# Optimization experiments

Measured on AMD Instinct MI355X. Metric: run time of the kernel, lower is better.

The kernel has to match this reference:

```python
import jax, jax.numpy as jnp
import numpy as np

# 1x1 conv (bias=False) + BatchNorm (eval mode, running mean=0, var=1 -> per-channel
# affine scale/shift, matching SyncBN at init/inference) + ReLU
def _cbr(x, W, g, b):
    y = jnp.einsum('bchw,oc->bohw', x, W)
    y = y * g[None, :, None, None] + b[None, :, None, None]
    return jax.nn.relu(y)


def setup_inputs() -> dict:
    key = jax.random.key(0)
    ks = jax.random.split(key, 8)
    B, C, H, Wd = 4, 512, 64, 64   # batch, feats_channels, spatial
    Ct = 256                        # transform_channels
    Ck = 2 * C                      # key_in_channels = feats_channels * 2

    def w(k, o, i):
        return jax.random.normal(k, (o, i), jnp.float32) * (1.0 / np.sqrt(i))

    inp = {"x": jax.random.normal(ks[0], (B, C, H, Wd), jnp.float32)}
    # query_project: two conv+BN+ReLU blocks, C -> Ct -> Ct
    inp["qW1"] = w(ks[1], Ct, C);  inp["qg1"] = jnp.ones((Ct,), jnp.float32); inp["qb1"] = jnp.zeros((Ct,), jnp.float32)
    inp["qW2"] = w(ks[2], Ct, Ct); inp["qg2"] = jnp.ones((Ct,), jnp.float32); inp["qb2"] = jnp.zeros((Ct,), jnp.float32)
    # key_project: two conv+BN+ReLU blocks, 2C -> Ct -> Ct
    inp["kW1"] = w(ks[3], Ct, Ck); inp["kg1"] = jnp.ones((Ct,), jnp.float32); inp["kb1"] = jnp.zeros((Ct,), jnp.float32)
    inp["kW2"] = w(ks[4], Ct, Ct); inp["kg2"] = jnp.ones((Ct,), jnp.float32); inp["kb2"] = jnp.zeros((Ct,), jnp.float32)
    # value_project: one conv+BN+ReLU, 2C -> Ct
    inp["vW"] = w(ks[5], Ct, Ck);  inp["vg"] = jnp.ones((Ct,), jnp.float32);  inp["vb"] = jnp.zeros((Ct,), jnp.float32)
    # out_project: one conv+BN+ReLU, Ct -> C
    inp["oW"] = w(ks[6], C, Ct);   inp["og"] = jnp.ones((C,), jnp.float32);   inp["ob"] = jnp.zeros((C,), jnp.float32)
    return inp


def reference(x, qW1, qg1, qb1, qW2, qg2, qb2,
              kW1, kg1, kb1, kW2, kg2, kb2,
              vW, vg, vb, oW, og, ob):
    B, C, H, W = x.shape
    # global avgpool to 1x1, bilinear-upsample back to HxW == broadcast of the mean
    xg = jnp.broadcast_to(jnp.mean(x, axis=(2, 3), keepdims=True), (B, C, H, W))
    key_feats = jnp.concatenate([xg, x], axis=1)  # [B, 2C, H, W]

    q = _cbr(_cbr(x, qW1, qg1, qb1), qW2, qg2, qb2)          # [B, Ct, H, W]
    k = _cbr(_cbr(key_feats, kW1, kg1, kb1), kW2, kg2, kb2)  # [B, Ct, H, W]
    v = _cbr(key_feats, vW, vg, vb)                          # [B, Ct, H, W]

    Ct = q.shape[1]
    HW = H * W
    qf = q.reshape(B, Ct, HW).transpose(0, 2, 1)  # [B, HW, Ct]
    kf = k.reshape(B, Ct, HW)                     # [B, Ct, HW]
    vf = v.reshape(B, Ct, HW).transpose(0, 2, 1)  # [B, HW, Ct]

    sim = jnp.einsum('bnc,bcm->bnm', qf, kf) * (Ct ** -0.5)  # [B, HW, HW]
    attn = jax.nn.softmax(sim, axis=-1)
    ctx = jnp.einsum('bnm,bmc->bnc', attn, vf)               # [B, HW, Ct]
    ctx = ctx.transpose(0, 2, 1).reshape(B, Ct, H, W)

    return _cbr(ctx, oW, og, ob)  # [B, C, H, W]
```

## Files before the change

### kernel.cpp

```cpp
#include <hip/hip_runtime.h>
#include <stdint.h>

typedef __bf16 bf16x8 __attribute__((ext_vector_type(8)));
typedef float f32x4 __attribute__((ext_vector_type(4)));
typedef unsigned short u16;
typedef uint32_t u32;

union V16 { uint4 v; u16 e[8]; };

__device__ __forceinline__ float bf2f(u16 h) {
    u32 u = ((u32)h) << 16; float f; __builtin_memcpy(&f, &u, 4); return f;
}
__device__ __forceinline__ u16 f2bf(float f) {
    u32 u; __builtin_memcpy(&u, &f, 4);
    u32 r = (u + 0x7FFFu + ((u >> 16) & 1u)) >> 16; return (u16)r;
}
__device__ __forceinline__ u32 cvtpk(float lo, float hi) {
    u32 r;
    asm("v_cvt_pk_bf16_f32 %0, %1, %2" : "=v"(r) : "v"(lo), "v"(hi));
    return r;
}
__device__ __forceinline__ f32x4 mfma16(bf16x8 a, bf16x8 b, f32x4 c) {
    return __builtin_amdgcn_mfma_f32_16x16x32_bf16(a, b, c, 0, 0, 0);
}
__device__ __forceinline__ void gll16(const u16* g, u16* l) {
    __builtin_amdgcn_global_load_lds(
        (const __attribute__((address_space(1))) unsigned int*)g,
        (__attribute__((address_space(3))) unsigned int*)l, 16, 0, 0);
}
__device__ __forceinline__ float loadElem(const void* p, size_t i, int fl) {
    if (fl == 1) return ((const float*)p)[i];
    if (fl == 2) return (float)((const double*)p)[i];
    return bf2f(((const u16*)p)[i]);
}

__global__ __launch_bounds__(256) void k_detect(const u32* __restrict__ xw, int* __restrict__ flag) {
    int t = threadIdx.x;
    int cA = 0, cB = 0;
    #pragma unroll
    for (int i = 0; i < 16; i++) {
        u32 w = xw[i * 256 + t];
        cA += (((w >> 23) & 0xFFu) >= 0xC0u) ? 1 : 0;
        cB += (((w >> 7)  & 0xFFu) >= 0xC0u) ? 1 : 0;
    }
    #pragma unroll
    for (int m = 32; m >= 1; m >>= 1) { cA += __shfl_xor(cA, m); cB += __shfl_xor(cB, m); }
    __shared__ int sA[4], sB[4];
    if ((t & 63) == 0) { sA[t >> 6] = cA; sB[t >> 6] = cB; }
    __syncthreads();
    if (t == 0) {
        int a = sA[0] + sA[1] + sA[2] + sA[3];
        int b = sB[0] + sB[1] + sB[2] + sB[3];
        *flag = (a > 64) ? 2 : ((b > 64) ? 1 : 0);
    }
}

__global__ __launch_bounds__(256) void k_xpose(const void* __restrict__ xv, const int* __restrict__ dt,
                                               u16* __restrict__ xT, float* __restrict__ partial) {
    __shared__ u16 tile[64][72];
    int b = blockIdx.z;
    int n0 = blockIdx.x * 64, c0 = blockIdx.y * 64;
    u16* xTb = xT + (size_t)b * 4096 * 512;
    int t = threadIdx.x;
    int fl = *dt;
    const size_t xbase = (size_t)b * 512 * 4096;
    if (fl == 1) {
        const float* xb = (const float*)xv + xbase;
        int cr = t >> 4, n4 = (t & 15) * 4;
        #pragma unroll
        for (int i = 0; i < 4; i++) {
            int c = cr + i * 16;
            float4 v = *reinterpret_cast<const float4*>(xb + (size_t)(c0 + c) * 4096 + n0 + n4);
            tile[n4 + 0][c] = f2bf(v.x); tile[n4 + 1][c] = f2bf(v.y);
            tile[n4 + 2][c] = f2bf(v.z); tile[n4 + 3][c] = f2bf(v.w);
            float s = (v.x + v.y) + (v.z + v.w);
            s += __shfl_xor(s, 1); s += __shfl_xor(s, 2);
            s += __shfl_xor(s, 4); s += __shfl_xor(s, 8);
            if ((t & 15) == 0)
                partial[((size_t)b * 512 + c0 + c) * 64 + blockIdx.x] = s;
        }
    } else {
        int c4 = t >> 6, n = t & 63;
        for (int i = 0; i < 16; i++) {
            int c = c4 + i * 4;
            float v = loadElem(xv, xbase + (size_t)(c0 + c) * 4096 + n0 + n, fl);
            tile[n][c] = f2bf(v);
            float s = v;
            #pragma unroll
            for (int m = 32; m >= 1; m >>= 1) s += __shfl_xor(s, m);
            if (n == 0)
                partial[((size_t)b * 512 + c0 + c) * 64 + blockIdx.x] = s;
        }
    }
    __syncthreads();
    int nr = t >> 3, c8 = (t & 7) * 8;
    #pragma unroll
    for (int i = 0; i < 2; i++) {
        int n = nr + i * 32;
        V16 v;
        #pragma unroll
        for (int j = 0; j < 8; j++) v.e[j] = tile[n][c8 + j];
        *reinterpret_cast<uint4*>(xTb + (size_t)(n0 + n) * 512 + c0 + c8) = v.v;
    }
}

__global__ __launch_bounds__(256) void k_mean2(const float* __restrict__ partial, float* __restrict__ xg) {
    int bc = blockIdx.x * 256 + threadIdx.x;
    const float* p = partial + (size_t)bc * 64;
    float s = 0.f;
    #pragma unroll
    for (int i = 0; i < 64; i++) s += p[i];
    xg[bc] = s * (1.f / 4096.f);
}

__global__ __launch_bounds__(64) void k_consts(const void* __restrict__ kW1, const void* __restrict__ vW,
                                               const int* __restrict__ dt, const float* __restrict__ xg,
                                               float* __restrict__ ck, float* __restrict__ cv) {
    int bo = blockIdx.x; int b = bo >> 8; int o = bo & 255;
    int l = threadIdx.x;
    int fl = *dt;
    const float* g = xg + b * 512;
    float sk = 0.f, sv = 0.f;
    for (int c = l; c < 512; c += 64) {
        float xv = g[c];
        sk += loadElem(kW1, (size_t)o * 1024 + c, fl) * xv;
        sv += loadElem(vW,  (size_t)o * 1024 + c, fl) * xv;
    }
    #pragma unroll
    for (int m = 32; m >= 1; m >>= 1) { sk += __shfl_xor(sk, m); sv += __shfl_xor(sv, m); }
    if (l == 0) { ck[bo] = sk; cv[bo] = sv; }
}

__global__ __launch_bounds__(256) void k_wconv(const void* __restrict__ qW1, const void* __restrict__ qW2,
                                               const void* __restrict__ kW1, const void* __restrict__ kW2,
                                               const void* __restrict__ vW, const void* __restrict__ oW,
                                               const int* __restrict__ dt, u16* __restrict__ dst) {
    int i = blockIdx.x * 256 + threadIdx.x;
    int fl = *dt;
    const void* s; size_t so;
    if (i < 131072)      { s = qW1; so = (size_t)i; }
    else if (i < 196608) { int j = i - 131072; s = qW2; so = (size_t)j; }
    else if (i < 327680) { int j = i - 196608; s = kW1; so = (size_t)(j >> 9) * 1024 + 512 + (j & 511); }
    else if (i < 393216) { int j = i - 327680; s = kW2; so = (size_t)j; }
    else if (i < 524288) { int j = i - 393216; s = vW;  so = (size_t)(j >> 9) * 1024 + 512 + (j & 511); }
    else                 { int j = i - 524288; s = oW;  so = (size_t)j; }
    dst[i] = f2bf(loadElem(s, so, fl));
}

__global__ __launch_bounds__(256) void k_pconv(const void* qg1, const void* qb1, const void* qg2, const void* qb2,
                                               const void* kg1, const void* kb1, const void* kg2, const void* kb2,
                                               const void* vg, const void* vb, const void* og, const void* ob,
                                               const int* __restrict__ dt, float* __restrict__ pg) {
    int j = blockIdx.x * 256 + threadIdx.x;
    if (j >= 3584) return;
    int fl = *dt;
    const void* s; int o;
    if (j < 256)       { s = qg1; o = j; }
    else if (j < 512)  { s = qb1; o = j - 256; }
    else if (j < 768)  { s = qg2; o = j - 512; }
    else if (j < 1024) { s = qb2; o = j - 768; }
    else if (j < 1280) { s = kg1; o = j - 1024; }
    else if (j < 1536) { s = kb1; o = j - 1280; }
    else if (j < 1792) { s = kg2; o = j - 1536; }
    else if (j < 2048) { s = kb2; o = j - 1792; }
    else if (j < 2304) { s = vg;  o = j - 2048; }
    else if (j < 2560) { s = vb;  o = j - 2304; }
    else if (j < 3072) { s = og;  o = j - 2560; }
    else               { s = ob;  o = j - 3072; }
    pg[j] = loadElem(s, (size_t)o, fl);
}

template<bool AFF_ROW, typename OT>
__global__ __launch_bounds__(256) void k_gemm_bt(
    const u16* __restrict__ A, long aBS, int lda,
    const u16* __restrict__ Bm, long bBS, int ldb,
    OT* __restrict__ C, long cBS, int ldc,
    const float* __restrict__ gamma, const float* __restrict__ beta,
    const float* __restrict__ bias, int biasBS, int K) {
    __shared__ u16 As[2][128 * 64];
    __shared__ u16 Bs[2][128 * 64];
    int b = blockIdx.z;
    const u16* Ab = A + (size_t)b * aBS;
    const u16* Bb = Bm + (size_t)b * bBS;
    OT* Cb = C + (size_t)b * cBS;
    int m0 = blockIdx.x * 128, n0 = blockIdx.y * 128;
    int t = threadIdx.x;
    int lane = t & 63, wid = t >> 6;
    int wr = wid >> 1, wc = wid & 1;
    int li = lane & 15, lk = lane >> 4;

    f32x4 acc[4][4] = {};

    auto stage = [&](int k0, int buf) {
        #pragma unroll
        for (int j = 0; j < 4; j++) {
            int c = wid * 4 + j;
            u32 pl = (u32)c * 1024 + (u32)lane * 16;
            u32 r = pl >> 7;
            u32 q = (pl & 127) ^ ((r & 7) << 4);
            gll16(Ab + (size_t)(m0 + r) * lda + k0 + (q >> 1), &As[buf][0] + (c << 9));
            gll16(Bb + (size_t)(n0 + r) * ldb + k0 + (q >> 1), &Bs[buf][0] + (c << 9));
        }
    };

    const int nk = K >> 6;
    stage(0, 0);

    for (int kst = 0; kst < nk; kst++) {
        int cur = kst & 1;
        if (kst + 1 < nk) {
            stage((kst + 1) << 6, cur ^ 1);
            asm volatile("s_waitcnt vmcnt(8)" ::: "memory");
        } else {
            asm volatile("s_waitcnt vmcnt(0)" ::: "memory");
        }
        __builtin_amdgcn_sched_barrier(0);
        __builtin_amdgcn_s_barrier();

        const char* AsB = (const char*)&As[cur][0];
        const char* BsB = (const char*)&Bs[cur][0];
        #pragma unroll
        for (int ks = 0; ks < 2; ks++) {
            bf16x8 af[4], bfr[4];
            #pragma unroll
            for (int mi = 0; mi < 4; mi++) {
                int r = wr * 64 + mi * 16 + li;
                u32 off = ((u32)(r * 128 + (ks * 32 + lk * 8) * 2)) ^ (((u32)(r & 7)) << 4);
                af[mi] = *reinterpret_cast<const bf16x8*>(AsB + off);
            }
            #pragma unroll
            for (int ni = 0; ni < 4; ni++) {
                int r = wc * 64 + ni * 16 + li;
                u32 off = ((u32)(r * 128 + (ks * 32 + lk * 8) * 2)) ^ (((u32)(r & 7)) << 4);
                bfr[ni] = *reinterpret_cast<const bf16x8*>(BsB + off);
            }
            #pragma unroll
            for (int mi = 0; mi < 4; mi++)
                #pragma unroll
                for (int ni = 0; ni < 4; ni++)
                    acc[mi][ni] = mfma16(af[mi], bfr[ni], acc[mi][ni]);
        }
        asm volatile("s_waitcnt lgkmcnt(0)" ::: "memory");
        __builtin_amdgcn_s_barrier();
    }
    #pragma unroll
    for (int mi = 0; mi < 4; mi++) {
        #pragma unroll
        for (int ni = 0; ni < 4; ni++) {
            #pragma unroll
            for (int r = 0; r < 4; r++) {
                int m = m0 + wr * 64 + mi * 16 + lk * 4 + r;
                int n = n0 + wc * 64 + ni * 16 + li;
                int oc = AFF_ROW ? m : n;
                float v = acc[mi][ni][r];
                if (bias) v += bias[b * biasBS + oc];
                float y = v * gamma[oc] + beta[oc];
                y = fmaxf(y, 0.f);
                if constexpr (sizeof(OT) == 2) Cb[(size_t)m * ldc + n] = f2bf(y);
                else                           Cb[(size_t)m * ldc + n] = y;
            }
        }
    }
}

__global__ __launch_bounds__(256) void k_gemm_tri(
    const u16* __restrict__ xT, long xBS,
    const u16* __restrict__ Wq, const u16* __restrict__ Wk, const u16* __restrict__ Wv,
    u16* __restrict__ Cq, u16* __restrict__ Ck2, u16* __restrict__ Cv, long cBS,
    const float* __restrict__ pg, const float* __restrict__ ckb, const float* __restrict__ cvb) {
    __shared__ u16 As[2][128 * 64];
    __shared__ u16 Bs[2][128 * 64];
    int z = blockIdx.z;
    int op = z >> 2, b = z & 3;
    const u16* Ab; const u16* Bb; u16* Cb; int ldc;
    const float* gamma; const float* beta; const float* bias;
    int m0, n0;
    if (op == 2) {
        Ab = Wv; Bb = xT + (size_t)b * xBS; Cb = Cv + (size_t)b * cBS; ldc = 4096;
        gamma = pg + 2048; beta = pg + 2304; bias = cvb;
        m0 = blockIdx.y * 128; n0 = blockIdx.x * 128;
    } else if (op == 1) {
        Ab = xT + (size_t)b * xBS; Bb = Wk; Cb = Ck2 + (size_t)b * cBS; ldc = 256;
        gamma = pg + 1024; beta = pg + 1280; bias = ckb;
        m0 = blockIdx.x * 128; n0 = blockIdx.y * 128;
    } else {
        Ab = xT + (size_t)b * xBS; Bb = Wq; Cb = Cq + (size_t)b * cBS; ldc = 256;
        gamma = pg + 0; beta = pg + 256; bias = nullptr;
        m0 = blockIdx.x * 128; n0 = blockIdx.y * 128;
    }
    int t = threadIdx.x;
    int lane = t & 63, wid = t >> 6;
    int wr = wid >> 1, wc = wid & 1;
    int li = lane & 15, lk = lane >> 4;

    f32x4 acc[4][4] = {};

    auto stage = [&](int k0, int buf) {
        #pragma unroll
        for (int j = 0; j < 4; j++) {
            int c = wid * 4 + j;
            u32 pl = (u32)c * 1024 + (u32)lane * 16;
            u32 r = pl >> 7;
            u32 q = (pl & 127) ^ ((r & 7) << 4);
            gll16(Ab + (size_t)(m0 + r) * 512 + k0 + (q >> 1), &As[buf][0] + (c << 9));
            gll16(Bb + (size_t)(n0 + r) * 512 + k0 + (q >> 1), &Bs[buf][0] + (c << 9));
        }
    };

    stage(0, 0);

    for (int kst = 0; kst < 8; kst++) {
        int cur = kst & 1;
        if (kst + 1 < 8) {
            stage((kst + 1) << 6, cur ^ 1);
            asm volatile("s_waitcnt vmcnt(8)" ::: "memory");
        } else {
            asm volatile("s_waitcnt vmcnt(0)" ::: "memory");
        }
        __builtin_amdgcn_sched_barrier(0);
        __builtin_amdgcn_s_barrier();

        const char* AsB = (const char*)&As[cur][0];
        const char* BsB = (const char*)&Bs[cur][0];
        #pragma unroll
        for (int ks = 0; ks < 2; ks++) {
            bf16x8 af[4], bfr[4];
            #pragma unroll
            for (int mi = 0; mi < 4; mi++) {
                int r = wr * 64 + mi * 16 + li;
                u32 off = ((u32)(r * 128 + (ks * 32 + lk * 8) * 2)) ^ (((u32)(r & 7)) << 4);
                af[mi] = *reinterpret_cast<const bf16x8*>(AsB + off);
            }
            #pragma unroll
            for (int ni = 0; ni < 4; ni++) {
                int r = wc * 64 + ni * 16 + li;
                u32 off = ((u32)(r * 128 + (ks * 32 + lk * 8) * 2)) ^ (((u32)(r & 7)) << 4);
                bfr[ni] = *reinterpret_cast<const bf16x8*>(BsB + off);
            }
            #pragma unroll
            for (int mi = 0; mi < 4; mi++)
                #pragma unroll
                for (int ni = 0; ni < 4; ni++)
                    acc[mi][ni] = mfma16(af[mi], bfr[ni], acc[mi][ni]);
        }
        asm volatile("s_waitcnt lgkmcnt(0)" ::: "memory");
        __builtin_amdgcn_s_barrier();
    }
    #pragma unroll
    for (int mi = 0; mi < 4; mi++) {
        #pragma unroll
        for (int ni = 0; ni < 4; ni++) {
            #pragma unroll
            for (int r = 0; r < 4; r++) {
                int m = m0 + wr * 64 + mi * 16 + lk * 4 + r;
                int n = n0 + wc * 64 + ni * 16 + li;
                int oc = (op == 2) ? m : n;
                float v = acc[mi][ni][r];
                if (bias) v += bias[b * 256 + oc];
                float y = v * gamma[oc] + beta[oc];
                y = fmaxf(y, 0.f);
                Cb[(size_t)m * ldc + n] = f2bf(y);
            }
        }
    }
}

__global__ __launch_bounds__(256) void k_gemm_pair(
    const u16* __restrict__ A0, const u16* __restrict__ A1, long aBS, int lda,
    const u16* __restrict__ B0, const u16* __restrict__ B1, int ldb,
    u16* __restrict__ C0, u16* __restrict__ C1, long cBS, int ldc,
    const float* __restrict__ g0, const float* __restrict__ be0,
    const float* __restrict__ g1, const float* __restrict__ be1, int K) {
    __shared__ u16 As[2][128 * 64];
    __shared__ u16 Bs[2][128 * 64];
    int z = blockIdx.z;
    int op = z >> 2, b = z & 3;
    const u16* Ab = (op ? A1 : A0) + (size_t)b * aBS;
    const u16* Bb = op ? B1 : B0;
    u16* Cb = (op ? C1 : C0) + (size_t)b * cBS;
    const float* gamma = op ? g1 : g0;
    const float* beta  = op ? be1 : be0;
    int m0 = blockIdx.x * 128, n0 = blockIdx.y * 128;
    int t = threadIdx.x;
    int lane = t & 63, wid = t >> 6;
    int wr = wid >> 1, wc = wid & 1;
    int li = lane & 15, lk = lane >> 4;

    f32x4 acc[4][4] = {};

    auto stage = [&](int k0, int buf) {
        #pragma unroll
        for (int j = 0; j < 4; j++) {
            int c = wid * 4 + j;
            u32 pl = (u32)c * 1024 + (u32)lane * 16;
            u32 r = pl >> 7;
            u32 q = (pl & 127) ^ ((r & 7) << 4);
            gll16(Ab + (size_t)(m0 + r) * lda + k0 + (q >> 1), &As[buf][0] + (c << 9));
            gll16(Bb + (size_t)(n0 + r) * ldb + k0 + (q >> 1), &Bs[buf][0] + (c << 9));
        }
    };

    const int nk = K >> 6;
    stage(0, 0);

    for (int kst = 0; kst < nk; kst++) {
        int cur = kst & 1;
        if (kst + 1 < nk) {
            stage((kst + 1) << 6, cur ^ 1);
            asm volatile("s_waitcnt vmcnt(8)" ::: "memory");
        } else {
            asm volatile("s_waitcnt vmcnt(0)" ::: "memory");
        }
        __builtin_amdgcn_sched_barrier(0);
        __builtin_amdgcn_s_barrier();

        const char* AsB = (const char*)&As[cur][0];
        const char* BsB = (const char*)&Bs[cur][0];
        #pragma unroll
        for (int ks = 0; ks < 2; ks++) {
            bf16x8 af[4], bfr[4];
            #pragma unroll
            for (int mi = 0; mi < 4; mi++) {
                int r = wr * 64 + mi * 16 + li;
                u32 off = ((u32)(r * 128 + (ks * 32 + lk * 8) * 2)) ^ (((u32)(r & 7)) << 4);
                af[mi] = *reinterpret_cast<const bf16x8*>(AsB + off);
            }
            #pragma unroll
            for (int ni = 0; ni < 4; ni++) {
                int r = wc * 64 + ni * 16 + li;
                u32 off = ((u32)(r * 128 + (ks * 32 + lk * 8) * 2)) ^ (((u32)(r & 7)) << 4);
                bfr[ni] = *reinterpret_cast<const bf16x8*>(BsB + off);
            }
            #pragma unroll
            for (int mi = 0; mi < 4; mi++)
                #pragma unroll
                for (int ni = 0; ni < 4; ni++)
                    acc[mi][ni] = mfma16(af[mi], bfr[ni], acc[mi][ni]);
        }
        asm volatile("s_waitcnt lgkmcnt(0)" ::: "memory");
        __builtin_amdgcn_s_barrier();
    }
    #pragma unroll
    for (int mi = 0; mi < 4; mi++) {
        #pragma unroll
        for (int ni = 0; ni < 4; ni++) {
            #pragma unroll
            for (int r = 0; r < 4; r++) {
                int m = m0 + wr * 64 + mi * 16 + lk * 4 + r;
                int n = n0 + wc * 64 + ni * 16 + li;
                float v = acc[mi][ni][r];
                float y = v * gamma[n] + beta[n];
                y = fmaxf(y, 0.f);
                Cb[(size_t)m * ldc + n] = f2bf(y);
            }
        }
    }
}

__global__ __launch_bounds__(256, 2) void k_attn(const u16* __restrict__ Q, const u16* __restrict__ Kt,
                                                 const u16* __restrict__ V, u16* __restrict__ Op,
                                                 float2* __restrict__ ML) {
    __shared__ u16 Ks[2][32 * 256];
    __shared__ u16 Vs[2][256 * 32];
    __shared__ u16 Ps[128 * 32];
    char* PsB = (char*)Ps;
    int wg = blockIdx.x;
    int bs = wg & 15, qt = wg >> 4;
    int b = bs >> 2, sp = bs & 3;
    int n0 = qt * 128;
    int k0 = sp * 1024;
    const size_t S = (size_t)4096 * 256;
    const u16* Qb = Q + (size_t)b * S + (size_t)n0 * 256;
    const u16* Kb = Kt + (size_t)b * S + (size_t)k0 * 256;
    const u16* Vb = V + (size_t)b * S + k0;
    int t = threadIdx.x;
    int lane = t & 63, wid = t >> 6;
    int li = lane & 15, lk = lane >> 4;
    int qw = wid * 32;

    bf16x8 qf[2][8];
    #pragma unroll
    for (int fq = 0; fq < 2; fq++)
        #pragma unroll
        for (int kc = 0; kc < 8; kc++)
            qf[fq][kc] = *reinterpret_cast<const bf16x8*>(Qb + (size_t)(qw + fq * 16 + li) * 256 + kc * 32 + lk * 8);

    f32x4 acc[2][16] = {};
    float M[2] = {-1e30f, -1e30f};
    float L[2] = {0.f, 0.f};
    const float SCL = 0.0625f * 1.44269504088896f;

    auto stage = [&](int kt, int buf) {
        const u16* Kp = Kb + (size_t)kt * 32 * 256;
        const u16* Vp = Vb + kt * 32;
        u16* Kd = &Ks[buf][0];
        u16* Vd = &Vs[buf][0];
        #pragma unroll
        for (int j = 0; j < 4; j++) {
            int c = wid * 4 + j;
            u32 pl = (u32)c * 1024 + (u32)lane * 16;
            u32 krow = pl >> 9;
            u32 kq = (pl & 511) ^ ((krow & 7) << 4);
            gll16(Kp + krow * 256 + (kq >> 1), Kd + (c << 9));
            u32 vcc = pl >> 6;
            u32 vq = (pl & 63) ^ (((vcc >> 1) & 3) << 4);
            gll16(Vp + (size_t)vcc * 4096 + (vq >> 1), Vd + (c << 9));
        }
    };

    stage(0, 0);

    for (int kt = 0; kt < 32; kt++) {
        int cur = kt & 1;
        if (kt + 1 < 32) {
            stage(kt + 1, cur ^ 1);
            asm volatile("s_waitcnt vmcnt(8)" ::: "memory");
        } else {
            asm volatile("s_waitcnt vmcnt(0)" ::: "memory");
        }
        __builtin_amdgcn_sched_barrier(0);
        __builtin_amdgcn_s_barrier();

        const char* KsB = (const char*)&Ks[cur][0];
        const char* VsB = (const char*)&Vs[cur][0];

        __builtin_amdgcn_s_setprio(1);
        f32x4 sf[2][2] = {};
        #pragma unroll
        for (int mk = 0; mk < 2; mk++) {
            #pragma unroll
            for (int kc = 0; kc < 8; kc++) {
                int row = mk * 16 + li;
                u32 off = (u32)(row * 512) + (((u32)(kc * 64 + lk * 16)) ^ (((u32)(row & 7)) << 4));
                bf16x8 kb = *reinterpret_cast<const bf16x8*>(KsB + off);
                sf[mk][0] = mfma16(kb, qf[0][kc], sf[mk][0]);
                sf[mk][1] = mfma16(kb, qf[1][kc], sf[mk][1]);
            }
        }
        __builtin_amdgcn_s_setprio(0);

        float lm[2];
        #pragma unroll
        for (int fq = 0; fq < 2; fq++) {
            lm[fq] = fmaxf(fmaxf(fmaxf(sf[0][fq][0], sf[0][fq][1]), fmaxf(sf[0][fq][2], sf[0][fq][3])),
                           fmaxf(fmaxf(sf[1][fq][0], sf[1][fq][1]), fmaxf(sf[1][fq][2], sf[1][fq][3]))) * SCL;
        }
        bool ok = (lm[0] <= M[0] + 24.f) && (lm[1] <= M[1] + 24.f);
        if (!__all(ok ? 1 : 0)) {
            #pragma unroll
            for (int fq = 0; fq < 2; fq++) {
                float mx = lm[fq];
                mx = fmaxf(mx, __shfl_xor(mx, 16));
                mx = fmaxf(mx, __shfl_xor(mx, 32));
                float nM = fmaxf(M[fq], mx);
                float rs = exp2f(M[fq] - nM);
                L[fq] *= rs; M[fq] = nM;
                #pragma unroll
                for (int ct = 0; ct < 16; ct++) {
                    acc[fq][ct][0] *= rs; acc[fq][ct][1] *= rs;
                    acc[fq][ct][2] *= rs; acc[fq][ct][3] *= rs;
                }
            }
        }
        #pragma unroll
        for (int fq = 0; fq < 2; fq++) {
            int row = qw + fq * 16 + li;
            float lloc = 0.f;
            #pragma unroll
            for (int mk = 0; mk < 2; mk++) {
                float p0 = exp2f(sf[mk][fq][0] * SCL - M[fq]);
                float p1 = exp2f(sf[mk][fq][1] * SCL - M[fq]);
                float p2 = exp2f(sf[mk][fq][2] * SCL - M[fq]);
                float p3 = exp2f(sf[mk][fq][3] * SCL - M[fq]);
                lloc += (p0 + p1) + (p2 + p3);
                uint2 pw; pw.x = cvtpk(p0, p1); pw.y = cvtpk(p2, p3);
                u32 off = ((u32)(row * 64 + mk * 32 + lk * 8)) ^ (((u32)(row & 7)) << 4);
                *reinterpret_cast<uint2*>(PsB + off) = pw;
            }
            L[fq] += lloc;
        }

        __builtin_amdgcn_s_setprio(1);
        {
            bf16x8 pb[2];
            #pragma unroll
            for (int fq = 0; fq < 2; fq++) {
                int row = qw + fq * 16 + li;
                u32 off = ((u32)(row * 64 + lk * 16)) ^ (((u32)(row & 7)) << 4);
                pb[fq] = *reinterpret_cast<const bf16x8*>(PsB + off);
            }
            #pragma unroll
            for (int ct = 0; ct < 16; ct++) {
                int vr = ct * 16 + li;
                u32 voff = (u32)(vr * 64) + (((u32)(lk * 16)) ^ (((u32)((vr >> 1) & 3)) << 4));
                bf16x8 va = *reinterpret_cast<const bf16x8*>(VsB + voff);
                acc[0][ct] = mfma16(va, pb[0], acc[0][ct]);
                acc[1][ct] = mfma16(va, pb[1], acc[1][ct]);
            }
        }
        __builtin_amdgcn_s_setprio(0);
        asm volatile("s_waitcnt lgkmcnt(0)" ::: "memory");
        __builtin_amdgcn_s_barrier();
    }

    #pragma unroll
    for (int fq = 0; fq < 2; fq++) {
        L[fq] += __shfl_xor(L[fq], 16);
        L[fq] += __shfl_xor(L[fq], 32);
    }

    size_t obase = (size_t)(sp * 4 + b) * 4096 + n0;
    #pragma unroll
    for (int fq = 0; fq < 2; fq++) {
        int q = qw + fq * 16 + li;
        #pragma unroll
        for (int ct = 0; ct < 16; ct++) {
            uint2 ow;
            ow.x = cvtpk(acc[fq][ct][0], acc[fq][ct][1]);
            ow.y = cvtpk(acc[fq][ct][2], acc[fq][ct][3]);
            *reinterpret_cast<uint2*>(&Op[(obase + q) * 256 + ct * 16 + lk * 4]) = ow;
        }
    }
    if (lk == 0) {
        #pragma unroll
        for (int fq = 0; fq < 2; fq++) {
            float2 v; v.x = M[fq]; v.y = L[fq];
            ML[obase + qw + fq * 16 + li] = v;
        }
    }
}

__global__ __launch_bounds__(256) void k_merge(const u16* __restrict__ Op, const float2* __restrict__ ML,
                                               u16* __restrict__ ctx) {
    int wg = blockIdx.x;
    int t = threadIdx.x;
    int b = wg >> 12, q = wg & 4095;
    float2 ml[4];
    float Mx = -1e30f;
    #pragma unroll
    for (int s = 0; s < 4; s++) { ml[s] = ML[((size_t)(s * 4 + b) << 12) + q]; Mx = fmaxf(Mx, ml[s].x); }
    float Lt = 0.f, w[4];
    #pragma unroll
    for (int s = 0; s < 4; s++) { w[s] = exp2f(ml[s].x - Mx); Lt += ml[s].y * w[s]; }
    float inv = 1.f / Lt;
    float o = 0.f;
    #pragma unroll
    for (int s = 0; s < 4; s++)
        o += w[s] * bf2f(Op[((((size_t)(s * 4 + b) << 12) + q)) * 256 + t]);
    ctx[(((size_t)b << 12) + q) * 256 + t] = f2bf(o * inv);
}

extern "C" void kernel_launch(void* const* d_in, const int* in_sizes, int n_in,
                              void* d_out, int out_size, void* d_ws, size_t ws_size,
                              hipStream_t stream) {
    const void* x   = d_in[0];
    const void* qW1 = d_in[1];  const void* qg1 = d_in[2];  const void* qb1 = d_in[3];
    const void* qW2 = d_in[4];  const void* qg2 = d_in[5];  const void* qb2 = d_in[6];
    const void* kW1 = d_in[7];  const void* kg1 = d_in[8];  const void* kb1 = d_in[9];
    const void* kW2 = d_in[10]; const void* kg2 = d_in[11]; const void* kb2 = d_in[12];
    const void* vW  = d_in[13]; const void* vg  = d_in[14]; const void* vb  = d_in[15];
    const void* oW  = d_in[16]; const void* og  = d_in[17]; const void* ob  = d_in[18];

    char* ws = (char*)d_ws;
    int*   dflag = (int*)ws;
    float* xg = (float*)(ws + 4096);
    float* ck = (float*)(ws + 16384);
    float* cv = (float*)(ws + 20480);
    float* pg = (float*)(ws + 24576);
    u16* wb = (u16*)(ws + 40960);
    u16* qW1b = wb;
    u16* qW2b = wb + 131072;
    u16* kW1b = wb + 196608;
    u16* kW2b = wb + 327680;
    u16* vWb  = wb + 393216;
    u16* oWb  = wb + 524288;
    float* partials = (float*)(ws + 0x180000);
    float2* mlBuf = (float2*)(ws + 0x200000);
    const size_t S = (size_t)4096 * 256;
    const size_t SLOT = 4 * S;
    u16* s0 = (u16*)(ws + 0x280000);
    u16* s1 = s0 + SLOT;
    u16* s2 = s1 + SLOT;
    u16* s3 = s2 + SLOT;
    u16* xT = (u16*)d_out;
    u16* k1buf = (u16*)d_out + 8388608;
    u16* opart = (u16*)d_out;
    u16* ctxBuf = s1;

    k_detect<<<1, 256, 0, stream>>>((const u32*)x, dflag);
    k_xpose<<<dim3(64, 8, 4), 256, 0, stream>>>(x, dflag, xT, partials);
    k_mean2<<<8, 256, 0, stream>>>(partials, xg);
    k_consts<<<1024, 64, 0, stream>>>(kW1, vW, dflag, xg, ck, cv);
    k_wconv<<<2560, 256, 0, stream>>>(qW1, qW2, kW1, kW2, vW, oW, dflag, wb);
    k_pconv<<<14, 256, 0, stream>>>(qg1, qb1, qg2, qb2, kg1, kb1, kg2, kb2,
                                    vg, vb, og, ob, dflag, pg);

    const long XS = (long)4096 * 512;
    k_gemm_tri<<<dim3(32, 2, 12), 256, 0, stream>>>(xT, XS, qW1b, kW1b, vWb,
        s0, k1buf, s3, (long)S, pg, ck, cv);
    k_gemm_pair<<<dim3(32, 2, 8), 256, 0, stream>>>(s0, k1buf, (long)S, 256,
        qW2b, kW2b, 256, s1, s2, (long)S, 256,
        pg + 512, pg + 768, pg + 1536, pg + 1792, 256);
    k_attn<<<512, 256, 0, stream>>>(s1, s2, s3, opart, mlBuf);
    k_merge<<<16384, 256, 0, stream>>>(opart, mlBuf, ctxBuf);
    k_gemm_bt<true, float><<<dim3(4, 32, 4), 256, 0, stream>>>(oWb, 0, 256, ctxBuf, (long)S, 256,
        (float*)d_out, (long)512 * 4096, 4096, pg + 2560, pg + 3072, nullptr, 0, 256);
}
```

Before: 215.7 us.

## Keep softmax probabilities in registers for PV MFMA and vectorize merge

The attention kernel no longer writes P to shared memory and reads it back. Each lane packs its own exp2 results directly into the bf16x8 B-operand. To keep the k-index mapping consistent, the V operand is now gathered as two 8-byte halves from the swizzled V tile. Separately, the merge kernel handles four channels per thread with 8-byte loads and stores over a quarter as many blocks. This removes an LDS round trip and a barrier-dependent buffer, but it doubles the V LDS load instructions and depends on the permuted k-order matching between P and V.

Measured after the change: 200.2 us. 1.08x faster.

```diff
diff --git a/kernel.cpp b/kernel.cpp
--- a/kernel.cpp
+++ b/kernel.cpp
@@ -7,6 +7,7 @@
 typedef uint32_t u32;
 
 union V16 { uint4 v; u16 e[8]; };
+union BF8 { uint4 u; bf16x8 v; };
 
 __device__ __forceinline__ float bf2f(u16 h) {
     u32 u = ((u32)h) << 16; float f; __builtin_memcpy(&f, &u, 4); return f;
@@ -462,8 +463,6 @@
                                                  float2* __restrict__ ML) {
     __shared__ u16 Ks[2][32 * 256];
     __shared__ u16 Vs[2][256 * 32];
-    __shared__ u16 Ps[128 * 32];
-    char* PsB = (char*)Ps;
     int wg = blockIdx.x;
     int bs = wg & 15, qt = wg >> 4;
     int b = bs >> 2, sp = bs & 3;
@@ -562,41 +561,39 @@
                 }
             }
         }
+
+        bf16x8 pb[2];
         #pragma unroll
         for (int fq = 0; fq < 2; fq++) {
-            int row = qw + fq * 16 + li;
-            float lloc = 0.f;
-            #pragma unroll
-            for (int mk = 0; mk < 2; mk++) {
-                float p0 = exp2f(sf[mk][fq][0] * SCL - M[fq]);
-                float p1 = exp2f(sf[mk][fq][1] * SCL - M[fq]);
-                float p2 = exp2f(sf[mk][fq][2] * SCL - M[fq]);
-                float p3 = exp2f(sf[mk][fq][3] * SCL - M[fq]);
-                lloc += (p0 + p1) + (p2 + p3);
-                uint2 pw; pw.x = cvtpk(p0, p1); pw.y = cvtpk(p2, p3);
-                u32 off = ((u32)(row * 64 + mk * 32 + lk * 8)) ^ (((u32)(row & 7)) << 4);
-                *reinterpret_cast<uint2*>(PsB + off) = pw;
-            }
-            L[fq] += lloc;
+            float p00 = exp2f(sf[0][fq][0] * SCL - M[fq]);
+            float p01 = exp2f(sf[0][fq][1] * SCL - M[fq]);
+            float p02 = exp2f(sf[0][fq][2] * SCL - M[fq]);
+            float p03 = exp2f(sf[0][fq][3] * SCL - M[fq]);
+            float p10 = exp2f(sf[1][fq][0] * SCL - M[fq]);
+            float p11 = exp2f(sf[1][fq][1] * SCL - M[fq]);
+            float p12 = exp2f(sf[1][fq][2] * SCL - M[fq]);
+            float p13 = exp2f(sf[1][fq][3] * SCL - M[fq]);
+            L[fq] += ((p00 + p01) + (p02 + p03)) + ((p10 + p11) + (p12 + p13));
+            BF8 pw;
+            pw.u.x = cvtpk(p00, p01);
+            pw.u.y = cvtpk(p02, p03);
+            pw.u.z = cvtpk(p10, p11);
+            pw.u.w = cvtpk(p12, p13);
+            pb[fq] = pw.v;
         }
 
         __builtin_amdgcn_s_setprio(1);
-        {
-            bf16x8 pb[2];
-            #pragma unroll
-            for (int fq = 0; fq < 2; fq++) {
-                int row = qw + fq * 16 + li;
-                u32 off = ((u32)(row * 64 + lk * 16)) ^ (((u32)(row & 7)) << 4);
-                pb[fq] = *reinterpret_cast<const bf16x8*>(PsB + off);
-            }
-            #pragma unroll
-            for (int ct = 0; ct < 16; ct++) {
-                int vr = ct * 16 + li;
-                u32 voff = (u32)(vr * 64) + (((u32)(lk * 16)) ^ (((u32)((vr >> 1) & 3)) << 4));
-                bf16x8 va = *reinterpret_cast<const bf16x8*>(VsB + voff);
-                acc[0][ct] = mfma16(va, pb[0], acc[0][ct]);
-                acc[1][ct] = mfma16(va, pb[1], acc[1][ct]);
-            }
+        #pragma unroll
+        for (int ct = 0; ct < 16; ct++) {
+            int vr = ct * 16 + li;
+            u32 sw = ((u32)((vr >> 1) & 3)) << 4;
+            u32 lo = (u32)(vr * 64) + (((u32)(lk * 8)) ^ sw);
+            u32 hi = (u32)(vr * 64) + (((u32)(32 + lk * 8)) ^ sw);
+            BF8 va;
+            *reinterpret_cast<uint2*>(&va.u.x) = *reinterpret_cast<const uint2*>(VsB + lo);
+            *reinterpret_cast<uint2*>(&va.u.z) = *reinterpret_cast<const uint2*>(VsB + hi);
+            acc[0][ct] = mfma16(va.v, pb[0], acc[0][ct]);
+            acc[1][ct] = mfma16(va.v, pb[1], acc[1][ct]);
         }
         __builtin_amdgcn_s_setprio(0);
         asm volatile("s_waitcnt lgkmcnt(0)" ::: "memory");
@@ -634,7 +631,9 @@
                                                u16* __restrict__ ctx) {
     int wg = blockIdx.x;
     int t = threadIdx.x;
-    int b = wg >> 12, q = wg & 4095;
+    int b = wg >> 10;
+    int q = (wg & 1023) * 4 + (t >> 6);
+    int c4 = (t & 63) * 4;
     float2 ml[4];
     float Mx = -1e30f;
     #pragma unroll
@@ -643,11 +642,19 @@
     #pragma unroll
     for (int s = 0; s < 4; s++) { w[s] = exp2f(ml[s].x - Mx); Lt += ml[s].y * w[s]; }
     float inv = 1.f / Lt;
-    float o = 0.f;
-    #pragma unroll
-    for (int s = 0; s < 4; s++)
-        o += w[s] * bf2f(Op[((((size_t)(s * 4 + b) << 12) + q)) * 256 + t]);
-    ctx[(((size_t)b << 12) + q) * 256 + t] = f2bf(o * inv);
+    float o0 = 0.f, o1 = 0.f, o2 = 0.f, o3 = 0.f;
+    #pragma unroll
+    for (int s = 0; s < 4; s++) {
+        uint2 v = *reinterpret_cast<const uint2*>(&Op[(((size_t)(s * 4 + b) << 12) + q) * 256 + c4]);
+        o0 += w[s] * bf2f((u16)(v.x & 0xFFFFu));
+        o1 += w[s] * bf2f((u16)(v.x >> 16));
+        o2 += w[s] * bf2f((u16)(v.y & 0xFFFFu));
+        o3 += w[s] * bf2f((u16)(v.y >> 16));
+    }
+    uint2 ow;
+    ow.x = cvtpk(o0 * inv, o1 * inv);
+    ow.y = cvtpk(o2 * inv, o3 * inv);
+    *reinterpret_cast<uint2*>(&ctx[(((size_t)b << 12) + q) * 256 + c4]) = ow;
 }
 
 extern "C" void kernel_launch(void* const* d_in, const int* in_sizes, int n_in,
@@ -702,7 +709,7 @@
         qW2b, kW2b, 256, s1, s2, (long)S, 256,
         pg + 512, pg + 768, pg + 1536, pg + 1792, 256);
     k_attn<<<512, 256, 0, stream>>>(s1, s2, s3, opart, mlBuf);
-    k_merge<<<16384, 256, 0, stream>>>(opart, mlBuf, ctxBuf);
+    k_merge<<<4096, 256, 0, stream>>>(opart, mlBuf, ctxBuf);
     k_gemm_bt<true, float><<<dim3(4, 32, 4), 256, 0, stream>>>(oWb, 0, 256, ctxBuf, (long)S, 256,
         (float*)d_out, (long)512 * 4096, 4096, pg + 2560, pg + 3072, nullptr, 0, 256);
 }
```
